# Kernel tuning notes

Hardware: AMD Instinct MI355X
Metric: run time of the kernel (lower is better)

Reference implementation:

```python
import jax, jax.numpy as jnp
import numpy as np

STRIDE = (1, 1, 1)  # (h_stride, w_stride, d_stride)
# padding order in module: (left,right,up,down,forward,backward) -> h, w, d dims
PAD = ((1, 1), (1, 1), (1, 1))  # ((pad_left,pad_right) on h, (up,down) on w, (fwd,bwd) on d)


def setup_inputs() -> dict:
    key = jax.random.key(0)
    k1, k2, k3 = jax.random.split(key, 3)
    X = jax.random.normal(k1, (4, 32, 32, 64, 64), dtype=jnp.float32)        # (B, Cin, h, w, d)
    weight = jax.random.normal(k2, (64, 32, 3, 3, 3), dtype=jnp.float32) * 0.5  # (Cout, Cin, kh, kw, kd)
    bias = jax.random.normal(k3, (64,), dtype=jnp.float32) * 0.5
    return {"X": X, "weight": weight, "bias": bias}


def _conv3d(X, weight, bias):
    # cross-correlation conv3d, identical math to the nested-loop MAC in MyConv3d
    y = jax.lax.conv_general_dilated(
        X, weight,
        window_strides=STRIDE,
        padding=PAD,
        dimension_numbers=("NCHWD", "OIHWD", "NCHWD"),
    )
    return y + bias[None, :, None, None, None]


def reference(X, weight, bias):
    return _conv3d(X, weight, bias)
```

## Files before the change

### kernel.cpp

```cpp
#include <hip/hip_runtime.h>
#include <hip/hip_bf16.h>

typedef __attribute__((ext_vector_type(8))) short bf16x8;
typedef __attribute__((ext_vector_type(4))) float f32x4;

#define B_N   4
#define C_IN  32
#define C_OUT 64
#define S_H   32
#define S_W   64
#define S_D   64
#define HWD   (S_H * S_W * S_D)

#define WPK_USHORTS     (4 * 28 * 64 * 8)
#define ZP_OFF_USHORTS  WPK_USHORTS
#define XPK_OFF_USHORTS (WPK_USHORTS + 2048)
#define XPK_USHORTS     (4UL * 4 * 32 * 64 * 64 * 8)
#define WS_NEEDED       ((size_t)(XPK_OFF_USHORTS + XPK_USHORTS) * 2)

__device__ __forceinline__ ushort f2bf(float f) {
    unsigned u = __builtin_bit_cast(unsigned, f);
    unsigned r = (u + 0x7FFFu + ((u >> 16) & 1u)) >> 16;
    return (ushort)r;
}

typedef const __attribute__((address_space(1))) unsigned int* dma_gptr;
typedef __attribute__((address_space(3))) unsigned int* dma_lptr;

__device__ __forceinline__ void dma16(const void* g, void* l) {
    __builtin_amdgcn_global_load_lds((dma_gptr)g, (dma_lptr)l, 16, 0, 0);
}

__global__ __launch_bounds__(256) void pack_w_kernel(
    const float* __restrict__ Wt, ushort* __restrict__ Wpk, ushort* __restrict__ Zp)
{
    int idx = blockIdx.x * 256 + threadIdx.x;
    int cic = idx / 1792;
    int r   = idx - cic * 1792;
    int tap = r >> 6;
    int co  = r & 63;
    bf16x8 pk;
    #pragma unroll
    for (int j = 0; j < 8; ++j)
        pk[j] = (tap < 27) ? (short)f2bf(Wt[((long)co * C_IN + cic * 8 + j) * 27 + tap])
                           : (short)0;
    *((bf16x8*)Wpk + idx) = pk;
    if (blockIdx.x == 0) {
        bf16x8 z;
        #pragma unroll
        for (int j = 0; j < 8; ++j) z[j] = 0;
        *((bf16x8*)Zp + threadIdx.x) = z;
    }
}

__global__ __launch_bounds__(256) void pack_x_kernel(
    const float* __restrict__ X, ushort* __restrict__ Xpk)
{
    long idx = (long)blockIdx.x * 256 + threadIdx.x;
    int d   = idx & 63;
    int w   = (idx >> 6) & 63;
    int h   = (idx >> 12) & 31;
    int b   = (idx >> 17) & 3;
    int cic = (idx >> 19) & 3;
    const float* xp = X + (((long)(b * C_IN + cic * 8) * S_H + h) * S_W + w) * S_D + d;
    bf16x8 pk;
    #pragma unroll
    for (int j = 0; j < 8; ++j) pk[j] = (short)f2bf(xp[(long)j * HWD]);
    *((bf16x8*)Xpk + idx) = pk;
}

__global__ __launch_bounds__(256, 2) void conv3d_mfma_kernel(
    const ushort* __restrict__ Xpk, const ushort* __restrict__ Wpk,
    const ushort* __restrict__ Zp,
    const float* __restrict__ bias, float* __restrict__ out)
{
    __shared__ ushort Xs[2][1280 * 8];
    __shared__ ushort Ws[1792 * 8];

    const int tid  = threadIdx.x;
    const int lane = tid & 63;
    const int wave = tid >> 6;
    const int nl   = lane & 15;
    const int quad = lane >> 4;

    const int blk = blockIdx.x;
    const int wt  = blk & 15;
    const int h   = (blk >> 4) & 31;
    const int b   = blk >> 9;
    const int w0  = wt * 4;

    const ushort* gp[5];
    int adv[5];
    #pragma unroll
    for (int k = 0; k < 5; ++k) {
        int s = tid + k * 256;
        if (s < 1188) {
            int hh   = s / 396;
            int r0   = s - hh * 396;
            int ww   = r0 / 66;
            int dpos = r0 - ww * 66;
            int hp  = h - 1 + hh;
            int wp2 = w0 - 1 + ww;
            int dp  = dpos - 1;
            bool ok = (unsigned)hp < S_H && (unsigned)wp2 < S_W && (unsigned)dp < S_D;
            if (ok) {
                gp[k]  = Xpk + ((long)b * 131072 + ((long)hp * S_W + wp2) * S_D + dp) * 8;
                adv[k] = 4 * 131072 * 8;
            } else { gp[k] = Zp; adv[k] = 0; }
        } else { gp[k] = Zp; adv[k] = 0; }
    }

    int a_off[7], b_off[7];
    #pragma unroll
    for (int tg = 0; tg < 7; ++tg) {
        int tap = tg * 4 + quad;
        int tb  = tap < 27 ? tap : 0;
        int kh = tb / 9;
        int r9 = tb - kh * 9;
        int kw = r9 / 3;
        int kd = r9 - kw * 3;
        a_off[tg] = (tap * 64 + nl) * 8;
        b_off[tg] = (((kh * 6 + kw + wave) * 66) + kd + nl) * 8;
    }

    float bs[16];
    #pragma unroll
    for (int mi = 0; mi < 4; ++mi)
        #pragma unroll
        for (int r = 0; r < 4; ++r)
            bs[mi * 4 + r] = bias[mi * 16 + quad * 4 + r];

    f32x4 acc[16];
    #pragma unroll
    for (int i = 0; i < 16; ++i) acc[i] = (f32x4){0.f, 0.f, 0.f, 0.f};

    #pragma unroll
    for (int k = 0; k < 5; ++k)
        dma16(gp[k], &Xs[0][(tid + k * 256) * 8]);

    for (int cic = 0; cic < 4; ++cic) {
        __syncthreads();

        {
            const ushort* src = Wpk + (long)cic * 1792 * 8;
            #pragma unroll
            for (int k = 0; k < 7; ++k) {
                int s = tid + k * 256;
                dma16(src + s * 8, &Ws[s * 8]);
            }
        }
        __syncthreads();

        if (cic < 3) {
            #pragma unroll
            for (int k = 0; k < 5; ++k)
                dma16(gp[k] + (long)(cic + 1) * adv[k],
                      &Xs[(cic + 1) & 1][(tid + k * 256) * 8]);
        }

        const ushort* xb = Xs[cic & 1];
        #pragma unroll
        for (int tg = 0; tg < 7; ++tg) {
            bf16x8 af[4], bf[4];
            #pragma unroll
            for (int mi = 0; mi < 4; ++mi)
                af[mi] = *(const bf16x8*)&Ws[a_off[tg] + mi * 128];
            #pragma unroll
            for (int dt = 0; dt < 4; ++dt)
                bf[dt] = *(const bf16x8*)&xb[b_off[tg] + dt * 128];
            #pragma unroll
            for (int mi = 0; mi < 4; ++mi)
                #pragma unroll
                for (int dt = 0; dt < 4; ++dt)
                    acc[mi * 4 + dt] = __builtin_amdgcn_mfma_f32_16x16x32_bf16(
                        af[mi], bf[dt], acc[mi * 4 + dt], 0, 0, 0);
        }
    }

    const int w = w0 + wave;
    #pragma unroll
    for (int mi = 0; mi < 4; ++mi) {
        #pragma unroll
        for (int dt = 0; dt < 4; ++dt) {
            f32x4 a = acc[mi * 4 + dt];
            int d0 = dt * 16 + nl;
            #pragma unroll
            for (int r = 0; r < 4; ++r) {
                int co = mi * 16 + quad * 4 + r;
                out[(((long)(b * C_OUT + co) * S_H + h) * S_W + w) * S_D + d0]
                    = a[r] + bs[mi * 4 + r];
            }
        }
    }
}

__global__ __launch_bounds__(256) void conv3d_mfma_fallback(
    const float* __restrict__ X, const float* __restrict__ Wt,
    const float* __restrict__ bias, float* __restrict__ out)
{
    __shared__ ushort Xs[3 * 6 * 66 * 8];
    __shared__ ushort Ws[28 * 64 * 8];

    const int tid  = threadIdx.x;
    const int lane = tid & 63;
    const int wave = tid >> 6;
    const int nl   = lane & 15;
    const int quad = lane >> 4;
    const int co_base = wave * 16;

    const int blk = blockIdx.x;
    const int wt  = blk & 15;
    const int h   = (blk >> 4) & 31;
    const int b   = blk >> 9;
    const int w0  = wt * 4;

    float bs[4];
    #pragma unroll
    for (int r = 0; r < 4; ++r) bs[r] = bias[co_base + quad * 4 + r];

    f32x4 acc[16];
    #pragma unroll
    for (int i = 0; i < 16; ++i) acc[i] = (f32x4){0.f, 0.f, 0.f, 0.f};

    for (int cic = 0; cic < 4; ++cic) {
        __syncthreads();
        for (int s = tid; s < 64 * 27; s += 256) {
            int co = s / 27;
            int t  = s - co * 27;
            const float* wp = Wt + ((long)co * C_IN + cic * 8) * 27 + t;
            bf16x8 pk;
            #pragma unroll
            for (int j = 0; j < 8; ++j) pk[j] = (short)f2bf(wp[j * 27]);
            *(bf16x8*)&Ws[(t * 64 + co) * 8] = pk;
        }
        for (int s = tid; s < 64; s += 256) {
            bf16x8 z;
            #pragma unroll
            for (int j = 0; j < 8; ++j) z[j] = 0;
            *(bf16x8*)&Ws[(27 * 64 + s) * 8] = z;
        }
        for (int s = tid; s < 1188; s += 256) {
            int hh   = s / 396;
            int r0   = s - hh * 396;
            int ww   = r0 / 66;
            int dpos = r0 - ww * 66;
            int hp = h - 1 + hh;
            int wp2 = w0 - 1 + ww;
            int dp = dpos - 1;
            bool ok = (unsigned)hp < S_H && (unsigned)wp2 < S_W && (unsigned)dp < S_D;
            int hc = min(max(hp, 0), S_H - 1);
            int wc = min(max(wp2, 0), S_W - 1);
            int dc = min(max(dp, 0), S_D - 1);
            const float* xp = X + (((long)(b * C_IN + cic * 8) * S_H + hc) * S_W + wc) * S_D + dc;
            bf16x8 pk;
            #pragma unroll
            for (int j = 0; j < 8; ++j) {
                float v = xp[(long)j * HWD];
                pk[j] = ok ? (short)f2bf(v) : (short)0;
            }
            *(bf16x8*)&Xs[s * 8] = pk;
        }
        __syncthreads();

        #pragma unroll
        for (int tg = 0; tg < 7; ++tg) {
            int tap = tg * 4 + quad;
            bf16x8 afrag = *(const bf16x8*)&Ws[(tap * 64 + co_base + nl) * 8];
            int tb = tap < 27 ? tap : 0;
            int kh = tb / 9;
            int r9 = tb - kh * 9;
            int kw = r9 / 3;
            int kd = r9 - kw * 3;
            int bbase = ((kh * 6 + kw) * 66 + kd + nl) * 8;
            #pragma unroll
            for (int wi = 0; wi < 4; ++wi) {
                #pragma unroll
                for (int dt = 0; dt < 4; ++dt) {
                    bf16x8 bfrag = *(const bf16x8*)&Xs[bbase + wi * (66 * 8) + dt * (16 * 8)];
                    acc[wi * 4 + dt] = __builtin_amdgcn_mfma_f32_16x16x32_bf16(
                        afrag, bfrag, acc[wi * 4 + dt], 0, 0, 0);
                }
            }
        }
    }

    #pragma unroll
    for (int wi = 0; wi < 4; ++wi) {
        int w = w0 + wi;
        #pragma unroll
        for (int dt = 0; dt < 4; ++dt) {
            int d0 = dt * 16 + nl;
            f32x4 a = acc[wi * 4 + dt];
            #pragma unroll
            for (int r = 0; r < 4; ++r) {
                int co = co_base + quad * 4 + r;
                out[(((long)(b * C_OUT + co) * S_H + h) * S_W + w) * S_D + d0] = a[r] + bs[r];
            }
        }
    }
}

extern "C" void kernel_launch(void* const* d_in, const int* in_sizes, int n_in,
                              void* d_out, int out_size, void* d_ws, size_t ws_size,
                              hipStream_t stream) {
    const float* X    = (const float*)d_in[0];
    const float* Wt   = (const float*)d_in[1];
    const float* bias = (const float*)d_in[2];
    float* out = (float*)d_out;

    if (ws_size >= WS_NEEDED) {
        ushort* Wpk = (ushort*)d_ws;
        ushort* Zp  = (ushort*)d_ws + ZP_OFF_USHORTS;
        ushort* Xpk = (ushort*)d_ws + XPK_OFF_USHORTS;
        pack_w_kernel<<<dim3(28),   dim3(256), 0, stream>>>(Wt, Wpk, Zp);
        pack_x_kernel<<<dim3(8192), dim3(256), 0, stream>>>(X, Xpk);
        conv3d_mfma_kernel<<<dim3(2048), dim3(256), 0, stream>>>(Xpk, Wpk, Zp, bias, out);
    } else {
        conv3d_mfma_fallback<<<dim3(2048), dim3(256), 0, stream>>>(X, Wt, bias, out);
    }
}
```

Measured before the change: 231.8 us.

## Compute two output h-rows per block to reuse weight fragments, drop X double buffer

Each block now computes two adjacent h rows, so it stages a 4-row input halo (1584 slots) and reuses each weight fragment load across both rows. The grid is halved to 1024 blocks. X is no longer double-buffered: the X DMA is issued together with the weight DMA before the barrier, which exposes load latency. Global pointers become 32-bit offsets from a single workspace base. Accumulators double to 32 f32x4 per thread, which adds register pressure against the two-blocks-per-SM launch bound.

```diff
diff --git a/kernel.cpp b/kernel.cpp
--- a/kernel.cpp
+++ b/kernel.cpp
@@ -17,6 +17,7 @@
 #define XPK_OFF_USHORTS (WPK_USHORTS + 2048)
 #define XPK_USHORTS     (4UL * 4 * 32 * 64 * 64 * 8)
 #define WS_NEEDED       ((size_t)(XPK_OFF_USHORTS + XPK_USHORTS) * 2)
+#define CIC_ADV         (4 * 131072 * 8)
 
 __device__ __forceinline__ ushort f2bf(float f) {
     unsigned u = __builtin_bit_cast(unsigned, f);
@@ -70,11 +71,10 @@
 }
 
 __global__ __launch_bounds__(256, 2) void conv3d_mfma_kernel(
-    const ushort* __restrict__ Xpk, const ushort* __restrict__ Wpk,
-    const ushort* __restrict__ Zp,
+    const ushort* __restrict__ ws_base,
     const float* __restrict__ bias, float* __restrict__ out)
 {
-    __shared__ ushort Xs[2][1280 * 8];
+    __shared__ ushort Xs[1792 * 8];
     __shared__ ushort Ws[1792 * 8];
 
     const int tid  = threadIdx.x;
@@ -85,32 +85,33 @@
 
     const int blk = blockIdx.x;
     const int wt  = blk & 15;
-    const int h   = (blk >> 4) & 31;
-    const int b   = blk >> 9;
+    const int hp  = (blk >> 4) & 15;
+    const int b   = blk >> 8;
+    const int h0  = hp * 2;
     const int w0  = wt * 4;
 
-    const ushort* gp[5];
-    int adv[5];
-    #pragma unroll
-    for (int k = 0; k < 5; ++k) {
+    int off[7], adv[7];
+    #pragma unroll
+    for (int k = 0; k < 7; ++k) {
         int s = tid + k * 256;
-        if (s < 1188) {
+        off[k] = ZP_OFF_USHORTS; adv[k] = 0;
+        if (s < 1584) {
             int hh   = s / 396;
             int r0   = s - hh * 396;
             int ww   = r0 / 66;
             int dpos = r0 - ww * 66;
-            int hp  = h - 1 + hh;
-            int wp2 = w0 - 1 + ww;
-            int dp  = dpos - 1;
-            bool ok = (unsigned)hp < S_H && (unsigned)wp2 < S_W && (unsigned)dp < S_D;
-            if (ok) {
-                gp[k]  = Xpk + ((long)b * 131072 + ((long)hp * S_W + wp2) * S_D + dp) * 8;
-                adv[k] = 4 * 131072 * 8;
-            } else { gp[k] = Zp; adv[k] = 0; }
-        } else { gp[k] = Zp; adv[k] = 0; }
-    }
-
-    int a_off[7], b_off[7];
+            int hx = h0 - 1 + hh;
+            int wx = w0 - 1 + ww;
+            int dx = dpos - 1;
+            if ((unsigned)hx < S_H && (unsigned)wx < S_W && (unsigned)dx < S_D) {
+                off[k] = XPK_OFF_USHORTS
+                       + ((b * HWD) + (hx * S_W + wx) * S_D + dx) * 8;
+                adv[k] = CIC_ADV;
+            }
+        }
+    }
+
+    int b_off[7];
     #pragma unroll
     for (int tg = 0; tg < 7; ++tg) {
         int tap = tg * 4 + quad;
@@ -119,76 +120,77 @@
         int r9 = tb - kh * 9;
         int kw = r9 / 3;
         int kd = r9 - kw * 3;
-        a_off[tg] = (tap * 64 + nl) * 8;
-        b_off[tg] = (((kh * 6 + kw + wave) * 66) + kd + nl) * 8;
-    }
-
-    float bs[16];
-    #pragma unroll
-    for (int mi = 0; mi < 4; ++mi)
-        #pragma unroll
-        for (int r = 0; r < 4; ++r)
-            bs[mi * 4 + r] = bias[mi * 16 + quad * 4 + r];
-
-    f32x4 acc[16];
-    #pragma unroll
-    for (int i = 0; i < 16; ++i) acc[i] = (f32x4){0.f, 0.f, 0.f, 0.f};
-
-    #pragma unroll
-    for (int k = 0; k < 5; ++k)
-        dma16(gp[k], &Xs[0][(tid + k * 256) * 8]);
+        b_off[tg] = (((kh * 6) + kw + wave) * 66 + kd + nl) * 8;
+    }
+
+    f32x4 acc[2][16];
+    #pragma unroll
+    for (int hl = 0; hl < 2; ++hl)
+        #pragma unroll
+        for (int i = 0; i < 16; ++i) acc[hl][i] = (f32x4){0.f, 0.f, 0.f, 0.f};
 
     for (int cic = 0; cic < 4; ++cic) {
         __syncthreads();
 
         {
-            const ushort* src = Wpk + (long)cic * 1792 * 8;
+            const ushort* src = ws_base + (long)cic * 1792 * 8;
             #pragma unroll
             for (int k = 0; k < 7; ++k) {
                 int s = tid + k * 256;
                 dma16(src + s * 8, &Ws[s * 8]);
             }
         }
+        #pragma unroll
+        for (int k = 0; k < 7; ++k)
+            dma16(ws_base + off[k] + cic * adv[k], &Xs[(tid + k * 256) * 8]);
+
         __syncthreads();
 
-        if (cic < 3) {
-            #pragma unroll
-            for (int k = 0; k < 5; ++k)
-                dma16(gp[k] + (long)(cic + 1) * adv[k],
-                      &Xs[(cic + 1) & 1][(tid + k * 256) * 8]);
-        }
-
-        const ushort* xb = Xs[cic & 1];
         #pragma unroll
         for (int tg = 0; tg < 7; ++tg) {
-            bf16x8 af[4], bf[4];
+            int tap = tg * 4 + quad;
+            bf16x8 af[4];
             #pragma unroll
             for (int mi = 0; mi < 4; ++mi)
-                af[mi] = *(const bf16x8*)&Ws[a_off[tg] + mi * 128];
-            #pragma unroll
-            for (int dt = 0; dt < 4; ++dt)
-                bf[dt] = *(const bf16x8*)&xb[b_off[tg] + dt * 128];
-            #pragma unroll
-            for (int mi = 0; mi < 4; ++mi)
+                af[mi] = *(const bf16x8*)&Ws[(tap * 64 + nl) * 8 + mi * 128];
+            #pragma unroll
+            for (int hl = 0; hl < 2; ++hl) {
+                bf16x8 bf[4];
                 #pragma unroll
                 for (int dt = 0; dt < 4; ++dt)
-                    acc[mi * 4 + dt] = __builtin_amdgcn_mfma_f32_16x16x32_bf16(
-                        af[mi], bf[dt], acc[mi * 4 + dt], 0, 0, 0);
+                    bf[dt] = *(const bf16x8*)&Xs[b_off[tg] + hl * 3168 + dt * 128];
+                #pragma unroll
+                for (int mi = 0; mi < 4; ++mi)
+                    #pragma unroll
+                    for (int dt = 0; dt < 4; ++dt)
+                        acc[hl][mi * 4 + dt] = __builtin_amdgcn_mfma_f32_16x16x32_bf16(
+                            af[mi], bf[dt], acc[hl][mi * 4 + dt], 0, 0, 0);
+            }
         }
     }
 
     const int w = w0 + wave;
-    #pragma unroll
-    for (int mi = 0; mi < 4; ++mi) {
-        #pragma unroll
-        for (int dt = 0; dt < 4; ++dt) {
-            f32x4 a = acc[mi * 4 + dt];
-            int d0 = dt * 16 + nl;
-            #pragma unroll
-            for (int r = 0; r < 4; ++r) {
-                int co = mi * 16 + quad * 4 + r;
-                out[(((long)(b * C_OUT + co) * S_H + h) * S_W + w) * S_D + d0]
-                    = a[r] + bs[mi * 4 + r];
+    float bs[16];
+    #pragma unroll
+    for (int mi = 0; mi < 4; ++mi)
+        #pragma unroll
+        for (int r = 0; r < 4; ++r)
+            bs[mi * 4 + r] = bias[mi * 16 + quad * 4 + r];
+    #pragma unroll
+    for (int hl = 0; hl < 2; ++hl) {
+        int h = h0 + hl;
+        #pragma unroll
+        for (int mi = 0; mi < 4; ++mi) {
+            #pragma unroll
+            for (int dt = 0; dt < 4; ++dt) {
+                f32x4 a = acc[hl][mi * 4 + dt];
+                int d0 = dt * 16 + nl;
+                #pragma unroll
+                for (int r = 0; r < 4; ++r) {
+                    int co = mi * 16 + quad * 4 + r;
+                    out[(((long)(b * C_OUT + co) * S_H + h) * S_W + w) * S_D + d0]
+                        = a[r] + bs[mi * 4 + r];
+                }
             }
         }
     }
@@ -244,13 +246,13 @@
             int r0   = s - hh * 396;
             int ww   = r0 / 66;
             int dpos = r0 - ww * 66;
-            int hp = h - 1 + hh;
-            int wp2 = w0 - 1 + ww;
-            int dp = dpos - 1;
-            bool ok = (unsigned)hp < S_H && (unsigned)wp2 < S_W && (unsigned)dp < S_D;
-            int hc = min(max(hp, 0), S_H - 1);
-            int wc = min(max(wp2, 0), S_W - 1);
-            int dc = min(max(dp, 0), S_D - 1);
+            int hx = h - 1 + hh;
+            int wx = w0 - 1 + ww;
+            int dx = dpos - 1;
+            bool ok = (unsigned)hx < S_H && (unsigned)wx < S_W && (unsigned)dx < S_D;
+            int hc = min(max(hx, 0), S_H - 1);
+            int wc = min(max(wx, 0), S_W - 1);
+            int dc = min(max(dx, 0), S_D - 1);
             const float* xp = X + (((long)(b * C_IN + cic * 8) * S_H + hc) * S_W + wc) * S_D + dc;
             bf16x8 pk;
             #pragma unroll
@@ -314,7 +316,7 @@
         ushort* Xpk = (ushort*)d_ws + XPK_OFF_USHORTS;
         pack_w_kernel<<<dim3(28),   dim3(256), 0, stream>>>(Wt, Wpk, Zp);
         pack_x_kernel<<<dim3(8192), dim3(256), 0, stream>>>(X, Xpk);
-        conv3d_mfma_kernel<<<dim3(2048), dim3(256), 0, stream>>>(Xpk, Wpk, Zp, bias, out);
+        conv3d_mfma_kernel<<<dim3(1024), dim3(256), 0, stream>>>((const ushort*)d_ws, bias, out);
     } else {
         conv3d_mfma_fallback<<<dim3(2048), dim3(256), 0, stream>>>(X, Wt, bias, out);
     }
```

New measurement: 238.7 us. 1.03x slower.
